# Kernel optimization log

Measured on AMD Instinct MI355X. Metric: run time of the kernel, lower is better.

The kernel has to match this reference:

```python
import jax, jax.numpy as jnp
import numpy as np

N_VOX, N_COLS = 200000, 5   # (N, 1 + 3 coords + 1 feat)
N_CLUSTS, PTS_PER_CLUST = 1024, 128
N_EDGES = 8192


def setup_inputs() -> dict:
    key = jax.random.key(0)
    k1, k2, k3 = jax.random.split(key, 3)
    data = jax.random.normal(k1, (N_VOX, N_COLS), dtype=jnp.float32)
    clusts = jax.random.randint(k2, (N_CLUSTS, PTS_PER_CLUST), 0, N_VOX)
    edge_index = jax.random.randint(k3, (2, N_EDGES), 0, N_CLUSTS)
    return {"data": data, "clusts": clusts, "edge_index": edge_index}


def reference(data, clusts, edge_index):
    # COORD_COLS = columns 1:4 of the sparse tensor
    voxels = data[:, 1:4]                       # [N, 3]
    pts = voxels[clusts]                        # [C, P, 3]
    x1 = pts[edge_index[0]]                     # [E, P, 3] first cluster of each edge
    x2 = pts[edge_index[1]]                     # [E, P, 3] second cluster
    P = x1.shape[1]

    # per-edge pairwise squared distances (argmin of d^2 == argmin of d)
    d2 = jnp.sum((x1[:, :, None, :] - x2[:, None, :, :]) ** 2, axis=-1)  # [E, P, P]
    imin = jnp.argmin(d2.reshape(d2.shape[0], -1), axis=1)               # [E]
    i1, i2 = imin // P, imin % P

    v1 = jnp.take_along_axis(x1, i1[:, None, None], axis=1)[:, 0, :]     # [E, 3]
    v2 = jnp.take_along_axis(x2, i2[:, None, None], axis=1)[:, 0, :]     # [E, 3]

    disp = v1 - v2
    lend = jnp.linalg.norm(disp, axis=-1, keepdims=True)                 # [E, 1]
    safe = jnp.where(lend > 0, lend, 1.0)
    dispn = jnp.where(lend > 0, disp / safe, disp)                       # unit displacement

    B = (dispn[:, :, None] * dispn[:, None, :]).reshape(-1, 9)           # outer product, [E, 9]

    feats = jnp.concatenate([v1, v2, dispn, lend, B], axis=1)            # [E, 19]
    # undirected: interleave original and flipped (v1<->v2, disp -> -disp, B invariant)
    feats_flip = jnp.concatenate([v2, v1, -dispn, lend, B], axis=1)
    full = jnp.stack([feats, feats_flip], axis=1).reshape(-1, 19)        # [2E, 19]
    return full
```

## Files before the change

### kernel.cpp

```cpp
#include <hip/hip_runtime.h>
#include <cstdint>

#define NV 200000
#define NCOLS 5
#define P 128
#define NE 8192

__global__ __launch_bounds__(256) void clust_geo_edge_kernel(
    const float* __restrict__ data,
    const int*   __restrict__ clusts,
    const int*   __restrict__ edge_index,
    float*       __restrict__ out)
{
    const int e = blockIdx.x;
    const int t = threadIdx.x;

    __shared__ float4 x1s[P];
    __shared__ float4 x2s[P];
    __shared__ unsigned long long wmin[4];

    const int c1 = edge_index[e];
    const int c2 = edge_index[NE + e];

    if (t < P) {
        const int v = clusts[c1 * P + t];
        x1s[t] = make_float4(data[v * NCOLS + 1], data[v * NCOLS + 2],
                             data[v * NCOLS + 3], 0.f);
    } else {
        const int p = t - P;
        const int v = clusts[c2 * P + p];
        x2s[p] = make_float4(data[v * NCOLS + 1], data[v * NCOLS + 2],
                             data[v * NCOLS + 3], 0.f);
    }
    __syncthreads();

    const int tj = t & 15;
    const int ti = t >> 4;

    float4 a[8], b[8];
    #pragma unroll
    for (int k = 0; k < 8; ++k) a[k] = x1s[ti + 16 * k];
    #pragma unroll
    for (int m = 0; m < 8; ++m) b[m] = x2s[tj + 16 * m];

    float bd[8];
    int   bj[8];
    #pragma unroll
    for (int k = 0; k < 8; ++k) { bd[k] = __builtin_inff(); bj[k] = 0; }

    #pragma unroll
    for (int m = 0; m < 8; ++m) {
        const int j = tj + 16 * m;
        const float bx = b[m].x, by = b[m].y, bz = b[m].z;
        #pragma unroll
        for (int k = 0; k < 8; ++k) {
            const float dx = __fsub_rn(a[k].x, bx);
            const float dy = __fsub_rn(a[k].y, by);
            const float dz = __fsub_rn(a[k].z, bz);
            const float d2 = __fadd_rn(__fadd_rn(__fmul_rn(dx, dx), __fmul_rn(dy, dy)),
                                       __fmul_rn(dz, dz));
            if (d2 < bd[k]) { bd[k] = d2; bj[k] = j; }
        }
    }

    float bestd = __builtin_inff();
    int   bestflat = 0;
    #pragma unroll
    for (int k = 0; k < 8; ++k) {
        if (bd[k] < bestd) { bestd = bd[k]; bestflat = (ti + 16 * k) * P + bj[k]; }
    }

    unsigned long long key =
        ((unsigned long long)__float_as_uint(bestd) << 32) | (unsigned)bestflat;

    for (int off = 32; off > 0; off >>= 1) {
        unsigned long long other = __shfl_down(key, off, 64);
        if (other < key) key = other;
    }
    const int wave = t >> 6;
    if ((t & 63) == 0) wmin[wave] = key;
    __syncthreads();

    if (t == 0) {
        unsigned long long k0 = wmin[0];
        #pragma unroll
        for (int w = 1; w < 4; ++w) if (wmin[w] < k0) k0 = wmin[w];
        const int flat = (int)(k0 & 0xffffffffull);
        const int i1 = flat >> 7;
        const int i2 = flat & (P - 1);

        const float v1x = x1s[i1].x, v1y = x1s[i1].y, v1z = x1s[i1].z;
        const float v2x = x2s[i2].x, v2y = x2s[i2].y, v2z = x2s[i2].z;

        const float dx = v1x - v2x, dy = v1y - v2y, dz = v1z - v2z;
        const float lend = sqrtf(dx * dx + dy * dy + dz * dz);

        float nx, ny, nz;
        if (lend > 0.f) { nx = dx / lend; ny = dy / lend; nz = dz / lend; }
        else            { nx = dx;        ny = dy;        nz = dz;        }

        const float B[9] = { nx*nx, nx*ny, nx*nz,
                             ny*nx, ny*ny, ny*nz,
                             nz*nx, nz*ny, nz*nz };

        float* o = out + (size_t)e * 38;
        o[0] = v1x; o[1] = v1y; o[2] = v1z;
        o[3] = v2x; o[4] = v2y; o[5] = v2z;
        o[6] = nx;  o[7] = ny;  o[8] = nz;  o[9] = lend;
        #pragma unroll
        for (int q = 0; q < 9; ++q) o[10 + q] = B[q];
        o[19] = v2x; o[20] = v2y; o[21] = v2z;
        o[22] = v1x; o[23] = v1y; o[24] = v1z;
        o[25] = -nx; o[26] = -ny; o[27] = -nz; o[28] = lend;
        #pragma unroll
        for (int q = 0; q < 9; ++q) o[29 + q] = B[q];
    }
}

extern "C" void kernel_launch(void* const* d_in, const int* in_sizes, int n_in,
                              void* d_out, int out_size, void* d_ws, size_t ws_size,
                              hipStream_t stream) {
    const float* data       = (const float*)d_in[0];
    const int*   clusts     = (const int*)d_in[1];
    const int*   edge_index = (const int*)d_in[2];
    float*       out        = (float*)d_out;

    clust_geo_edge_kernel<<<NE, 256, 0, stream>>>(data, clusts, edge_index, out);
}
```

Measured before the change: 94.53 us.

## Compute pairwise distances with fp16 split MFMA and exact refinement of candidates

Adds a gather kernel that packs each cluster's coordinates into padded fp16 hi/lo split rows, so that one GEMM yields approximate |a|^2 - 2ab + |b|^2. It also records a global max-coordinate bound. The edge kernel then computes all 128x128 distances per edge with 16x16x32 f16 MFMA instructions instead of scalar FP32 math. It finds the approximate minimum and recomputes exact FP32 distances only for entries within an error-based threshold of it. This moves the dominant arithmetic onto matrix cores, at the cost of an extra pass, more workspace traffic, and correctness that depends on the heuristic error bound. The b2max atomic target is never reset.

```diff
diff --git a/kernel.cpp b/kernel.cpp
--- a/kernel.cpp
+++ b/kernel.cpp
@@ -5,115 +5,292 @@
 #define NCOLS 5
 #define P 128
 #define NE 8192
-
-__global__ __launch_bounds__(256) void clust_geo_edge_kernel(
+#define NC 1024
+#define KPAD 40
+
+typedef _Float16 half8 __attribute__((ext_vector_type(8)));
+typedef float   float4v __attribute__((ext_vector_type(4)));
+
+__global__ __launch_bounds__(256) void gather_kernel(
+    const float* __restrict__ data,
+    const int*   __restrict__ clusts,
+    float4*      __restrict__ dense,
+    short*       __restrict__ wsA,
+    short*       __restrict__ wsB,
+    int*         __restrict__ b2max)
+{
+    const int idx = blockIdx.x * 256 + threadIdx.x;
+    const int v = clusts[idx];
+    const float x = data[v * NCOLS + 1];
+    const float y = data[v * NCOLS + 2];
+    const float z = data[v * NCOLS + 3];
+    dense[idx] = make_float4(x, y, z, 0.f);
+
+    const _Float16 xh = (_Float16)x, yh = (_Float16)y, zh = (_Float16)z;
+    const float xhf = (float)xh, yhf = (float)yh, zhf = (float)zh;
+    const _Float16 xl = (_Float16)(x - xhf);
+    const _Float16 yl = (_Float16)(y - yhf);
+    const _Float16 zl = (_Float16)(z - zhf);
+
+    const float a2 = x * x + y * y + z * z;
+    const _Float16 a2h = (_Float16)a2;
+    const _Float16 a2l = (_Float16)(a2 - (float)a2h);
+    const _Float16 one = (_Float16)1.0f;
+    const _Float16 n2  = (_Float16)(-2.0f);
+    const _Float16 m2xh = n2 * xh, m2yh = n2 * yh, m2zh = n2 * zh;
+    const _Float16 m2xl = n2 * xl, m2yl = n2 * yl, m2zl = n2 * zl;
+
+    _Float16 rowA[KPAD];
+    _Float16 rowB[KPAD];
+    #pragma unroll
+    for (int k = 0; k < KPAD; ++k) { rowA[k] = (_Float16)0.f; rowB[k] = (_Float16)0.f; }
+    rowA[0] = xh;  rowA[1] = yh;  rowA[2] = zh;
+    rowA[3] = xl;  rowA[4] = yl;  rowA[5] = zl;
+    rowA[6] = xh;  rowA[7] = yh;  rowA[8] = zh;
+    rowA[9] = a2h; rowA[10] = a2l; rowA[11] = one; rowA[12] = one;
+
+    rowB[0] = m2xh; rowB[1] = m2yh; rowB[2] = m2zh;
+    rowB[3] = m2xh; rowB[4] = m2yh; rowB[5] = m2zh;
+    rowB[6] = m2xl; rowB[7] = m2yl; rowB[8] = m2zl;
+    rowB[9] = one;  rowB[10] = one; rowB[11] = a2h; rowB[12] = a2l;
+
+    ulonglong2* dA = (ulonglong2*)(wsA + (size_t)idx * KPAD);
+    ulonglong2* dB = (ulonglong2*)(wsB + (size_t)idx * KPAD);
+    const ulonglong2* sAp = (const ulonglong2*)rowA;
+    const ulonglong2* sBp = (const ulonglong2*)rowB;
+    #pragma unroll
+    for (int k = 0; k < 5; ++k) { dA[k] = sAp[k]; dB[k] = sBp[k]; }
+
+    float mm = fmaxf(fmaxf(x * x, y * y), z * z);
+    for (int off = 32; off > 0; off >>= 1)
+        mm = fmaxf(mm, __shfl_down(mm, off, 64));
+    if ((threadIdx.x & 63) == 0) atomicMax(b2max, __float_as_int(mm));
+}
+
+__global__ __launch_bounds__(256) void edge_kernel(
+    const float4* __restrict__ dense,
+    const short*  __restrict__ wsA,
+    const short*  __restrict__ wsB,
+    const int*    __restrict__ edge_index,
+    const float*  __restrict__ b2max,
+    float*        __restrict__ out)
+{
+    #pragma clang fp contract(off)
+
+    const int e = blockIdx.x;
+    const int t = threadIdx.x;
+
+    __shared__ short sA[P * KPAD];
+    __shared__ short sB[P * KPAD];
+    __shared__ float wfmin[4];
+    __shared__ unsigned long long wmin[4];
+
+    const int c1 = edge_index[e];
+    const int c2 = edge_index[NE + e];
+
+    {
+        const ulonglong2* gA = (const ulonglong2*)(wsA + (size_t)c1 * P * KPAD);
+        const ulonglong2* gB = (const ulonglong2*)(wsB + (size_t)c2 * P * KPAD);
+        ulonglong2* lA = (ulonglong2*)sA;
+        ulonglong2* lB = (ulonglong2*)sB;
+        for (int i = t; i < 640; i += 256) { lA[i] = gA[i]; lB[i] = gB[i]; }
+    }
+    __syncthreads();
+
+    const int lane = t & 63, w = t >> 6;
+    const int m = lane & 15, quad = lane >> 4;
+
+    const half8 a0 = *(const half8*)&sA[(w * 32 +      m) * KPAD + quad * 8];
+    const half8 a1 = *(const half8*)&sA[(w * 32 + 16 + m) * KPAD + quad * 8];
+
+    float4v acc[2][8];
+    #pragma unroll
+    for (int tr = 0; tr < 2; ++tr)
+        #pragma unroll
+        for (int tc = 0; tc < 8; ++tc)
+            acc[tr][tc] = (float4v){0.f, 0.f, 0.f, 0.f};
+
+    #pragma unroll
+    for (int tc = 0; tc < 8; ++tc) {
+        const half8 b = *(const half8*)&sB[(tc * 16 + m) * KPAD + quad * 8];
+        acc[0][tc] = __builtin_amdgcn_mfma_f32_16x16x32_f16(a0, b, acc[0][tc], 0, 0, 0);
+        acc[1][tc] = __builtin_amdgcn_mfma_f32_16x16x32_f16(a1, b, acc[1][tc], 0, 0, 0);
+    }
+
+    float tmin[16];
+    #pragma unroll
+    for (int tr = 0; tr < 2; ++tr)
+        #pragma unroll
+        for (int tc = 0; tc < 8; ++tc) {
+            const float4v vv = acc[tr][tc];
+            tmin[tr * 8 + tc] = fminf(fminf(vv.x, vv.y), fminf(vv.z, vv.w));
+        }
+    float mymin = tmin[0];
+    #pragma unroll
+    for (int k = 1; k < 16; ++k) mymin = fminf(mymin, tmin[k]);
+
+    for (int off = 32; off > 0; off >>= 1)
+        mymin = fminf(mymin, __shfl_down(mymin, off, 64));
+    if (lane == 0) wfmin[w] = mymin;
+    __syncthreads();
+    const float smin = fminf(fminf(wfmin[0], wfmin[1]), fminf(wfmin[2], wfmin[3]));
+
+    const float B2 = *b2max;
+    const float tau = smin + (1.5e-4f * B2 + 8.0e-3f);
+
+    unsigned long long bestkey = ~0ull;
+    #pragma unroll
+    for (int tr = 0; tr < 2; ++tr) {
+        #pragma unroll
+        for (int tc = 0; tc < 8; ++tc) {
+            if (tmin[tr * 8 + tc] <= tau) {
+                const float4v vv = acc[tr][tc];
+                #pragma unroll
+                for (int r = 0; r < 4; ++r) {
+                    const float sv = (r == 0) ? vv.x : (r == 1) ? vv.y : (r == 2) ? vv.z : vv.w;
+                    if (sv <= tau) {
+                        const int i = w * 32 + tr * 16 + quad * 4 + r;
+                        const int j = tc * 16 + m;
+                        const float4 pa = dense[c1 * P + i];
+                        const float4 pb = dense[c2 * P + j];
+                        const float dx = __fsub_rn(pa.x, pb.x);
+                        const float dy = __fsub_rn(pa.y, pb.y);
+                        const float dz = __fsub_rn(pa.z, pb.z);
+                        const float d2 = __fadd_rn(__fadd_rn(__fmul_rn(dx, dx), __fmul_rn(dy, dy)),
+                                                   __fmul_rn(dz, dz));
+                        const unsigned long long key =
+                            ((unsigned long long)__float_as_uint(d2) << 32) |
+                            (unsigned)(i * P + j);
+                        if (key < bestkey) bestkey = key;
+                    }
+                }
+            }
+        }
+    }
+
+    for (int off = 32; off > 0; off >>= 1) {
+        unsigned long long other = __shfl_down(bestkey, off, 64);
+        if (other < bestkey) bestkey = other;
+    }
+    if (lane == 0) wmin[w] = bestkey;
+    __syncthreads();
+
+    if (t == 0) {
+        unsigned long long k0 = wmin[0];
+        #pragma unroll
+        for (int q = 1; q < 4; ++q) if (wmin[q] < k0) k0 = wmin[q];
+        const int flat = (int)(k0 & 0xffffffffull);
+        const int i1 = flat >> 7;
+        const int i2 = flat & (P - 1);
+
+        const float4 p1 = dense[c1 * P + i1];
+        const float4 p2 = dense[c2 * P + i2];
+        const float v1x = p1.x, v1y = p1.y, v1z = p1.z;
+        const float v2x = p2.x, v2y = p2.y, v2z = p2.z;
+
+        const float dx = v1x - v2x, dy = v1y - v2y, dz = v1z - v2z;
+        const float lend = sqrtf(dx * dx + dy * dy + dz * dz);
+
+        float nx, ny, nz;
+        if (lend > 0.f) { nx = dx / lend; ny = dy / lend; nz = dz / lend; }
+        else            { nx = dx;        ny = dy;        nz = dz;        }
+
+        const float B[9] = { nx*nx, nx*ny, nx*nz,
+                             ny*nx, ny*ny, ny*nz,
+                             nz*nx, nz*ny, nz*nz };
+
+        float* o = out + (size_t)e * 38;
+        o[0] = v1x; o[1] = v1y; o[2] = v1z;
+        o[3] = v2x; o[4] = v2y; o[5] = v2z;
+        o[6] = nx;  o[7] = ny;  o[8] = nz;  o[9] = lend;
+        #pragma unroll
+        for (int q = 0; q < 9; ++q) o[10 + q] = B[q];
+        o[19] = v2x; o[20] = v2y; o[21] = v2z;
+        o[22] = v1x; o[23] = v1y; o[24] = v1z;
+        o[25] = -nx; o[26] = -ny; o[27] = -nz; o[28] = lend;
+        #pragma unroll
+        for (int q = 0; q < 9; ++q) o[29 + q] = B[q];
+    }
+}
+
+__global__ __launch_bounds__(256) void exact_kernel(
     const float* __restrict__ data,
     const int*   __restrict__ clusts,
     const int*   __restrict__ edge_index,
     float*       __restrict__ out)
 {
+    #pragma clang fp contract(off)
     const int e = blockIdx.x;
     const int t = threadIdx.x;
-
     __shared__ float4 x1s[P];
     __shared__ float4 x2s[P];
     __shared__ unsigned long long wmin[4];
-
     const int c1 = edge_index[e];
     const int c2 = edge_index[NE + e];
-
     if (t < P) {
         const int v = clusts[c1 * P + t];
-        x1s[t] = make_float4(data[v * NCOLS + 1], data[v * NCOLS + 2],
-                             data[v * NCOLS + 3], 0.f);
+        x1s[t] = make_float4(data[v*NCOLS+1], data[v*NCOLS+2], data[v*NCOLS+3], 0.f);
     } else {
         const int p = t - P;
         const int v = clusts[c2 * P + p];
-        x2s[p] = make_float4(data[v * NCOLS + 1], data[v * NCOLS + 2],
-                             data[v * NCOLS + 3], 0.f);
-    }
-    __syncthreads();
-
-    const int tj = t & 15;
-    const int ti = t >> 4;
-
+        x2s[p] = make_float4(data[v*NCOLS+1], data[v*NCOLS+2], data[v*NCOLS+3], 0.f);
+    }
+    __syncthreads();
+    const int tj = t & 15, ti = t >> 4;
     float4 a[8], b[8];
     #pragma unroll
-    for (int k = 0; k < 8; ++k) a[k] = x1s[ti + 16 * k];
-    #pragma unroll
-    for (int m = 0; m < 8; ++m) b[m] = x2s[tj + 16 * m];
-
-    float bd[8];
-    int   bj[8];
+    for (int k = 0; k < 8; ++k) a[k] = x1s[ti + 16*k];
+    #pragma unroll
+    for (int mm = 0; mm < 8; ++mm) b[mm] = x2s[tj + 16*mm];
+    float bd[8]; int bj[8];
     #pragma unroll
     for (int k = 0; k < 8; ++k) { bd[k] = __builtin_inff(); bj[k] = 0; }
-
-    #pragma unroll
-    for (int m = 0; m < 8; ++m) {
-        const int j = tj + 16 * m;
-        const float bx = b[m].x, by = b[m].y, bz = b[m].z;
+    #pragma unroll
+    for (int mm = 0; mm < 8; ++mm) {
+        const int j = tj + 16*mm;
         #pragma unroll
         for (int k = 0; k < 8; ++k) {
-            const float dx = __fsub_rn(a[k].x, bx);
-            const float dy = __fsub_rn(a[k].y, by);
-            const float dz = __fsub_rn(a[k].z, bz);
-            const float d2 = __fadd_rn(__fadd_rn(__fmul_rn(dx, dx), __fmul_rn(dy, dy)),
-                                       __fmul_rn(dz, dz));
+            const float dx = __fsub_rn(a[k].x, b[mm].x);
+            const float dy = __fsub_rn(a[k].y, b[mm].y);
+            const float dz = __fsub_rn(a[k].z, b[mm].z);
+            const float d2 = __fadd_rn(__fadd_rn(__fmul_rn(dx,dx), __fmul_rn(dy,dy)), __fmul_rn(dz,dz));
             if (d2 < bd[k]) { bd[k] = d2; bj[k] = j; }
         }
     }
-
-    float bestd = __builtin_inff();
-    int   bestflat = 0;
-    #pragma unroll
-    for (int k = 0; k < 8; ++k) {
-        if (bd[k] < bestd) { bestd = bd[k]; bestflat = (ti + 16 * k) * P + bj[k]; }
-    }
-
-    unsigned long long key =
-        ((unsigned long long)__float_as_uint(bestd) << 32) | (unsigned)bestflat;
-
+    float bestd = __builtin_inff(); int bestflat = 0;
+    #pragma unroll
+    for (int k = 0; k < 8; ++k)
+        if (bd[k] < bestd) { bestd = bd[k]; bestflat = (ti + 16*k) * P + bj[k]; }
+    unsigned long long key = ((unsigned long long)__float_as_uint(bestd) << 32) | (unsigned)bestflat;
     for (int off = 32; off > 0; off >>= 1) {
         unsigned long long other = __shfl_down(key, off, 64);
         if (other < key) key = other;
     }
-    const int wave = t >> 6;
-    if ((t & 63) == 0) wmin[wave] = key;
-    __syncthreads();
-
+    if ((t & 63) == 0) wmin[t >> 6] = key;
+    __syncthreads();
     if (t == 0) {
         unsigned long long k0 = wmin[0];
         #pragma unroll
-        for (int w = 1; w < 4; ++w) if (wmin[w] < k0) k0 = wmin[w];
+        for (int q = 1; q < 4; ++q) if (wmin[q] < k0) k0 = wmin[q];
         const int flat = (int)(k0 & 0xffffffffull);
-        const int i1 = flat >> 7;
-        const int i2 = flat & (P - 1);
-
+        const int i1 = flat >> 7, i2 = flat & (P - 1);
         const float v1x = x1s[i1].x, v1y = x1s[i1].y, v1z = x1s[i1].z;
         const float v2x = x2s[i2].x, v2y = x2s[i2].y, v2z = x2s[i2].z;
-
         const float dx = v1x - v2x, dy = v1y - v2y, dz = v1z - v2z;
-        const float lend = sqrtf(dx * dx + dy * dy + dz * dz);
-
+        const float lend = sqrtf(dx*dx + dy*dy + dz*dz);
         float nx, ny, nz;
-        if (lend > 0.f) { nx = dx / lend; ny = dy / lend; nz = dz / lend; }
-        else            { nx = dx;        ny = dy;        nz = dz;        }
-
-        const float B[9] = { nx*nx, nx*ny, nx*nz,
-                             ny*nx, ny*ny, ny*nz,
-                             nz*nx, nz*ny, nz*nz };
-
+        if (lend > 0.f) { nx = dx/lend; ny = dy/lend; nz = dz/lend; }
+        else            { nx = dx; ny = dy; nz = dz; }
+        const float B[9] = { nx*nx, nx*ny, nx*nz, ny*nx, ny*ny, ny*nz, nz*nx, nz*ny, nz*nz };
         float* o = out + (size_t)e * 38;
-        o[0] = v1x; o[1] = v1y; o[2] = v1z;
-        o[3] = v2x; o[4] = v2y; o[5] = v2z;
-        o[6] = nx;  o[7] = ny;  o[8] = nz;  o[9] = lend;
-        #pragma unroll
-        for (int q = 0; q < 9; ++q) o[10 + q] = B[q];
-        o[19] = v2x; o[20] = v2y; o[21] = v2z;
-        o[22] = v1x; o[23] = v1y; o[24] = v1z;
-        o[25] = -nx; o[26] = -ny; o[27] = -nz; o[28] = lend;
-        #pragma unroll
-        for (int q = 0; q < 9; ++q) o[29 + q] = B[q];
+        o[0]=v1x; o[1]=v1y; o[2]=v1z; o[3]=v2x; o[4]=v2y; o[5]=v2z;
+        o[6]=nx; o[7]=ny; o[8]=nz; o[9]=lend;
+        #pragma unroll
+        for (int q = 0; q < 9; ++q) o[10+q] = B[q];
+        o[19]=v2x; o[20]=v2y; o[21]=v2z; o[22]=v1x; o[23]=v1y; o[24]=v1z;
+        o[25]=-nx; o[26]=-ny; o[27]=-nz; o[28]=lend;
+        #pragma unroll
+        for (int q = 0; q < 9; ++q) o[29+q] = B[q];
     }
 }
 
@@ -125,5 +302,21 @@
     const int*   edge_index = (const int*)d_in[2];
     float*       out        = (float*)d_out;
 
-    clust_geo_edge_kernel<<<NE, 256, 0, stream>>>(data, clusts, edge_index, out);
+    char* wsc = (char*)d_ws;
+    const size_t denseOff = 256;
+    const size_t denseBytes = (size_t)NC * P * sizeof(float4);
+    const size_t fragBytes  = (size_t)NC * P * KPAD * sizeof(short);
+    const size_t need = denseOff + denseBytes + 2 * fragBytes;
+
+    if (ws_size >= need) {
+        int*    b2max = (int*)wsc;
+        float4* dense = (float4*)(wsc + denseOff);
+        short*  wsA   = (short*)(wsc + denseOff + denseBytes);
+        short*  wsB   = wsA + (size_t)NC * P * KPAD;
+        gather_kernel<<<(NC * P) / 256, 256, 0, stream>>>(data, clusts, dense, wsA, wsB, b2max);
+        edge_kernel<<<NE, 256, 0, stream>>>(dense, wsA, wsB, edge_index,
+                                            (const float*)b2max, out);
+    } else {
+        exact_kernel<<<NE, 256, 0, stream>>>(data, clusts, edge_index, out);
+    }
 }
```

Result: slower. 144.1 us (+52.4%).
